# Kernel optimization log

Measured on AMD Instinct MI355X. Metric: run time of the kernel, lower is better.

## Reference

```python
import jax, jax.numpy as jnp
import numpy as np

N_QUBITS = 6
Q_DEPTH = 2
K = 3
PAD = 1
EPS = 1e-9
Q_DIM = 2 ** N_QUBITS


def _rx(t):
    c = jnp.cos(t / 2).astype(jnp.complex64)
    s = jnp.sin(t / 2).astype(jnp.complex64)
    return jnp.stack([jnp.stack([c, -1j * s]), jnp.stack([-1j * s, c])])


def _ry(t):
    c = jnp.cos(t / 2).astype(jnp.complex64)
    s = jnp.sin(t / 2).astype(jnp.complex64)
    return jnp.stack([jnp.stack([c, -s]), jnp.stack([s, c])])


def _u3(t, p, lm):
    c = jnp.cos(t / 2).astype(jnp.complex64)
    s = jnp.sin(t / 2).astype(jnp.complex64)
    ep = jnp.exp(1j * p.astype(jnp.complex64))
    el = jnp.exp(1j * lm.astype(jnp.complex64))
    return jnp.stack([jnp.stack([c, -el * s]), jnp.stack([ep * s, ep * el * c])])


def _apply_1q(st, U, wire):
    # st: (bsz, 2**n) complex; wire 0 = most significant bit (torchquantum layout)
    s = st.reshape(-1, 2 ** wire, 2, 2 ** (N_QUBITS - wire - 1))
    s = jnp.einsum('ab,nxby->nxay', U, s)
    return s.reshape(-1, Q_DIM)


def _apply_cnot(st, wire):
    # CNOT with control=wire, target=wire+1 (adjacent)
    s = st.reshape(-1, 2 ** wire, 2, 2, 2 ** (N_QUBITS - wire - 2))
    s = jnp.stack([s[:, :, 0], s[:, :, 1, ::-1]], axis=2)
    return s.reshape(-1, Q_DIM)


def _quantum_forward(x, inp_scale, in_proj_w, in_proj_b, weights, meas_w, out_proj_w, out_proj_b):
    B, C, H, W = x.shape
    # Unfold(kernel=3, pad=1, stride=1) -> (B, C*9, H*W), channel-major then (kh, kw)
    xp = jnp.pad(x, ((0, 0), (0, 0), (PAD, PAD), (PAD, PAD)))
    pat = jnp.stack([xp[:, :, i:i + H, j:j + W] for i in range(K) for j in range(K)], axis=2)
    pat = pat.reshape(B, C * K * K, H * W).transpose(0, 2, 1).reshape(-1, C * K * K)
    pf = pat * inp_scale
    xq = pf @ in_proj_w.T + in_proj_b                       # (bsz, 64)
    xq = xq / (jnp.linalg.norm(xq, axis=-1, keepdims=True) + EPS)
    st = xq.astype(jnp.complex64)                           # (bsz, 2**n)
    for l in range(Q_DEPTH):
        for i in range(N_QUBITS):
            st = _apply_1q(st, _rx(weights[l, i, 0]), i)
            st = _apply_1q(st, _ry(weights[l, i, 1]), i)
        for i in range(N_QUBITS - 1):
            st = _apply_cnot(st, i)
        for i in range(N_QUBITS):
            st = _apply_1q(st, _ry(weights[l, i, 2]), i)
    for i in range(N_QUBITS):
        st = _apply_1q(st, _u3(meas_w[i, 0], meas_w[i, 1], meas_w[i, 2]), i)
    probs = st.real ** 2 + st.imag ** 2                     # |amp|^2
    out = probs @ out_proj_w.T + out_proj_b                 # (bsz, out_channels)
    return out.reshape(B, H * W, -1).transpose(0, 2, 1).reshape(B, -1, H, W)


def setup_inputs() -> dict:
    key = jax.random.key(0)
    ks = jax.random.split(key, 8)
    C_IN, C_OUT = 32, 64
    patch_dim = C_IN * K * K  # 288
    x = jax.random.normal(ks[0], (16, C_IN, 64, 64), dtype=jnp.float32)
    inp_scale = jnp.ones((patch_dim,), dtype=jnp.float32)
    in_proj_w = jax.random.normal(ks[1], (Q_DIM, patch_dim), dtype=jnp.float32) / np.sqrt(patch_dim)
    in_proj_b = jax.random.normal(ks[2], (Q_DIM,), dtype=jnp.float32) / np.sqrt(patch_dim)
    weights = 0.1 * jax.random.normal(ks[3], (Q_DEPTH, N_QUBITS, 3), dtype=jnp.float32)
    meas_w = 0.1 * jax.random.normal(ks[4], (N_QUBITS, 3), dtype=jnp.float32)
    out_proj_w = jax.random.normal(ks[5], (C_OUT, Q_DIM), dtype=jnp.float32) / np.sqrt(Q_DIM)
    out_proj_b = jax.random.normal(ks[6], (C_OUT,), dtype=jnp.float32) / np.sqrt(Q_DIM)
    return {"x": x, "inp_scale": inp_scale, "in_proj_w": in_proj_w, "in_proj_b": in_proj_b,
            "weights": weights, "meas_w": meas_w, "out_proj_w": out_proj_w, "out_proj_b": out_proj_b}


def reference(x, inp_scale, in_proj_w, in_proj_b, weights, meas_w, out_proj_w, out_proj_b):
    return _quantum_forward(x, inp_scale, in_proj_w, in_proj_b, weights, meas_w, out_proj_w, out_proj_b)
```

## Files before the change

kernel.cpp:

```cpp
#include <hip/hip_runtime.h>

typedef float f32x4 __attribute__((ext_vector_type(4)));
typedef short bf16x8 __attribute__((ext_vector_type(8)));

#define NB   16
#define CIN  32
#define HW   64
#define CKK  288
#define QD   64

#define WS_WSF 0
#define WS_MCF 18432
#define WS_WOF 26624
#define WS_XQF 30720

__device__ __forceinline__ unsigned short f2bf(float f) {
  unsigned u = __builtin_bit_cast(unsigned, f);
  u += 0x7FFFu + ((u >> 16) & 1u);
  return (unsigned short)(u >> 16);
}

struct C2 { float r, i; };
struct M2 { C2 a, b, c, d; };

__device__ __forceinline__ C2 cmul(C2 x, C2 y) { return { x.r*y.r - x.i*y.i, x.r*y.i + x.i*y.r }; }
__device__ __forceinline__ C2 cadd(C2 x, C2 y) { return { x.r + y.r, x.i + y.i }; }
__device__ __forceinline__ M2 mmul(M2 X, M2 Y) {
  return { cadd(cmul(X.a, Y.a), cmul(X.b, Y.c)),
           cadd(cmul(X.a, Y.b), cmul(X.b, Y.d)),
           cadd(cmul(X.c, Y.a), cmul(X.d, Y.c)),
           cadd(cmul(X.c, Y.b), cmul(X.d, Y.d)) };
}

__device__ __forceinline__ M2 mRX(float t) {
  float s, c; __sincosf(t * 0.5f, &s, &c);
  return { {c,0.f}, {0.f,-s}, {0.f,-s}, {c,0.f} };
}
__device__ __forceinline__ M2 mRY(float t) {
  float s, c; __sincosf(t * 0.5f, &s, &c);
  return { {c,0.f}, {-s,0.f}, {s,0.f}, {c,0.f} };
}
__device__ __forceinline__ M2 mU3(float t, float p, float lm) {
  float s, c; __sincosf(t * 0.5f, &s, &c);
  float sp, cp; __sincosf(p, &sp, &cp);
  float sl, cl; __sincosf(lm, &sl, &cl);
  float spl, cpl; __sincosf(p + lm, &spl, &cpl);
  return { {c,0.f}, {-cl*s, -sl*s}, {cp*s, sp*s}, {cpl*c, spl*c} };
}

__global__ __launch_bounds__(256) void prep_kernel(
    const float* __restrict__ x,
    const float* __restrict__ in_proj_w, const float* __restrict__ inp_scale,
    const float* __restrict__ weights, const float* __restrict__ meas_w,
    const float* __restrict__ out_proj_w, unsigned short* __restrict__ ws)
{
  const int tid = threadIdx.x, blk = blockIdx.x;

  if (blk < 1024) {
    const int b = blk >> 6, y = blk & 63;
    const int lane = tid & 63, w = tid >> 6;
    const float* src = x + ((b * CIN + w * 8) * HW + y) * HW + lane;
    unsigned short* dst = ws + WS_XQF + (size_t)((b * HW + y) * HW + lane) * CIN + w * 8;
    bf16x8 o8;
#pragma unroll
    for (int j = 0; j < 8; ++j) o8[j] = (short)f2bf(src[j * HW * HW]);
    *(bf16x8*)dst = o8;
    return;
  }
  const int blk2 = blk - 1024;

  if (blk2 < 36) {
    int f = blk2, kk = f >> 2, jt = f & 3;
#pragma unroll
    for (int u = 0; u < 2; ++u) {
      int r = tid * 2 + u;
      int lw = r >> 3, e = r & 7;
      int row = jt * 16 + (lw & 15);
      int ch = (lw >> 4) * 8 + e;
      int src = ch * 9 + kk;
      ws[WS_WSF + f * 512 + r] = f2bf(in_proj_w[row * CKK + src] * inp_scale[src]);
    }
    return;
  }
  if (blk2 == 36) {
#pragma unroll
    for (int m = 0; m < 16; ++m) {
      int d = tid * 16 + m;
      int f = d >> 9, r = d & 511;
      int lw = r >> 3, e = r & 7;
      int kk = f >> 2, ot = f & 3;
      int src = (ot * 16 + (lw & 15)) * 64 + kk * 32 + (lw >> 4) * 8 + e;
      ws[WS_WOF + d] = f2bf(out_proj_w[src]);
    }
    return;
  }

  const int lane = tid & 63, wid = tid >> 6;
  const int col = (blk2 - 37) * 4 + wid;

  float re, im;
  {
    C2 amp = {1.f, 0.f};
#pragma unroll
    for (int q = 0; q < 6; ++q) {
      M2 G = mmul(mRY(weights[q * 3 + 1]), mRX(weights[q * 3 + 0]));
      int rb = (lane >> (5 - q)) & 1;
      int cb = (col >> (5 - q)) & 1;
      C2 sel = rb ? (cb ? G.d : G.c) : (cb ? G.b : G.a);
      amp = cmul(amp, sel);
    }
    re = amp.r; im = amp.i;
  }

  const int t1 = (lane ^ (lane >> 1) ^ (lane >> 2) ^ (lane >> 3) ^ (lane >> 4) ^ (lane >> 5)) & 63;
  const int t2 = (lane ^ (lane >> 2) ^ (lane >> 4)) & 63;

  auto applyM = [&](int maskShuf, int rb, M2 U) {
    float arr = rb ? U.d.r : U.a.r, ari = rb ? U.d.i : U.a.i;
    float brr = rb ? U.c.r : U.b.r, bri = rb ? U.c.i : U.b.i;
    float pre = __shfl_xor(re, maskShuf);
    float pim = __shfl_xor(im, maskShuf);
    float nr = arr * re - ari * im + brr * pre - bri * pim;
    float ni = arr * im + ari * re + brr * pim + bri * pre;
    re = nr; im = ni;
  };

  const int MK1[6] = {0x01, 0x03, 0x06, 0x0C, 0x18, 0x30};
  const int MK2[6] = {0x01, 0x02, 0x05, 0x0A, 0x14, 0x28};

#pragma unroll
  for (int q = 0; q < 6; ++q) {
    const int b = 5 - q;
    M2 U = mmul(mmul(mRY(weights[18 + q * 3 + 1]), mRX(weights[18 + q * 3 + 0])),
                mRY(weights[q * 3 + 2]));
    applyM(MK1[b], (t1 >> b) & 1, U);
  }
#pragma unroll
  for (int q = 0; q < 6; ++q) {
    const int b = 5 - q;
    M2 U = mmul(mU3(meas_w[q * 3], meas_w[q * 3 + 1], meas_w[q * 3 + 2]),
                mRY(weights[18 + q * 3 + 2]));
    applyM(MK2[b], (t2 >> b) & 1, U);
  }

  unsigned short* McF = ws + WS_MCF;
  const int nRe = t2 >> 4, c16r = t2 & 15;
  const int kk = col >> 5, gc = (col >> 3) & 3, e = col & 7;
  const int off = (gc * 16 + c16r) * 8 + e;
  McF[(kk * 8 + nRe) * 512 + off]     = f2bf(re);
  McF[(kk * 8 + 4 + nRe) * 512 + off] = f2bf(im);
}

#define LDA 72
#define LDO 65

__global__ __launch_bounds__(256) void main_kernel(
    const float* __restrict__ b_in, const float* __restrict__ b_out,
    const unsigned short* __restrict__ ws, float* __restrict__ out)
{
  __shared__ __align__(16) unsigned char smem[18432];
  unsigned short* a_lds = (unsigned short*)smem;
  unsigned short* p_lds = (unsigned short*)(smem + 9216);
  float* o_lds = (float*)smem;

  const int tid = threadIdx.x, lane = tid & 63, wid = tid >> 6;
  const int g = lane >> 4, c16 = lane & 15;
  const int blk = (blockIdx.x & 7) * 128 + (blockIdx.x >> 3);
  const int b = blk >> 6, h = blk & 63;

  const unsigned short* WsF = ws + WS_WSF;
  const unsigned short* McF = ws + WS_MCF;
  const unsigned short* WoF = ws + WS_WOF;
  const unsigned short* xqb = ws + WS_XQF + (size_t)b * (HW * HW * CIN);

  f32x4 acc[4];
#pragma unroll
  for (int jt = 0; jt < 4; ++jt) { float bi = b_in[jt * 16 + c16]; acc[jt] = f32x4{bi, bi, bi, bi}; }

  const int ar = wid * 16 + c16;
  const int xw0 = (ar >= 1) ? ar - 1 : 0;
  const int xw2 = (ar <= 62) ? ar + 1 : 63;
  const bool ok0 = (ar >= 1), ok2 = (ar <= 62);

#pragma unroll
  for (int kk = 0; kk < 9; ++kk) {
    const int di = kk / 3, dj = kk % 3;
    const int y = h + di - 1;
    bf16x8 af;
    if ((unsigned)y < 64u) {
      const int xwc = (dj == 0) ? xw0 : (dj == 1) ? ar : xw2;
      af = *(const bf16x8*)(xqb + (y * 64 + xwc) * CIN + g * 8);
      const bool okx = (dj == 0) ? ok0 : (dj == 1) ? true : ok2;
      if (!okx)
#pragma unroll
        for (int i = 0; i < 8; ++i) af[i] = 0;
    } else {
#pragma unroll
      for (int i = 0; i < 8; ++i) af[i] = 0;
    }
#pragma unroll
    for (int jt = 0; jt < 4; ++jt) {
      bf16x8 bf_ = *(const bf16x8*)(WsF + (kk * 4 + jt) * 512 + lane * 8);
      acc[jt] = __builtin_amdgcn_mfma_f32_16x16x32_bf16(af, bf_, acc[jt], 0, 0, 0);
    }
  }

  float s[4];
#pragma unroll
  for (int r = 0; r < 4; ++r) {
    float t = acc[0][r] * acc[0][r] + acc[1][r] * acc[1][r] +
              acc[2][r] * acc[2][r] + acc[3][r] * acc[3][r];
    t += __shfl_xor(t, 1); t += __shfl_xor(t, 2); t += __shfl_xor(t, 4); t += __shfl_xor(t, 8);
    s[r] = 1.f / (sqrtf(t) + 1e-9f);
  }
#pragma unroll
  for (int jt = 0; jt < 4; ++jt)
#pragma unroll
    for (int r = 0; r < 4; ++r)
      a_lds[(wid * 16 + g * 4 + r) * LDA + jt * 16 + c16] = f2bf(acc[jt][r] * s[r]);

  f32x4 uv[8];
#pragma unroll
  for (int n = 0; n < 8; ++n) uv[n] = f32x4{0.f, 0.f, 0.f, 0.f};
#pragma unroll
  for (int kk = 0; kk < 2; ++kk) {
    bf16x8 af = *(const bf16x8*)(a_lds + (wid * 16 + c16) * LDA + kk * 32 + g * 8);
#pragma unroll
    for (int n = 0; n < 8; ++n) {
      bf16x8 bf_ = *(const bf16x8*)(McF + (kk * 8 + n) * 512 + lane * 8);
      uv[n] = __builtin_amdgcn_mfma_f32_16x16x32_bf16(af, bf_, uv[n], 0, 0, 0);
    }
  }

#pragma unroll
  for (int n = 0; n < 4; ++n)
#pragma unroll
    for (int r = 0; r < 4; ++r) {
      float p = uv[n][r] * uv[n][r] + uv[n + 4][r] * uv[n + 4][r];
      p_lds[(wid * 16 + g * 4 + r) * LDA + n * 16 + c16] = f2bf(p);
    }

  f32x4 o[4];
#pragma unroll
  for (int ot = 0; ot < 4; ++ot) { float bo = b_out[ot * 16 + c16]; o[ot] = f32x4{bo, bo, bo, bo}; }
#pragma unroll
  for (int kk = 0; kk < 2; ++kk) {
    bf16x8 af = *(const bf16x8*)(p_lds + (wid * 16 + c16) * LDA + kk * 32 + g * 8);
#pragma unroll
    for (int ot = 0; ot < 4; ++ot) {
      bf16x8 bf_ = *(const bf16x8*)(WoF + (kk * 4 + ot) * 512 + lane * 8);
      o[ot] = __builtin_amdgcn_mfma_f32_16x16x32_bf16(af, bf_, o[ot], 0, 0, 0);
    }
  }

  __syncthreads();
#pragma unroll
  for (int ot = 0; ot < 4; ++ot)
#pragma unroll
    for (int r = 0; r < 4; ++r)
      o_lds[(ot * 16 + c16) * LDO + wid * 16 + g * 4 + r] = o[ot][r];
  __syncthreads();

  float* outb = out + (size_t)b * QD * HW * HW + h * HW;
#pragma unroll
  for (int it = 0; it < 16; ++it) {
    int orow = it * 4 + wid;
    outb[orow * (HW * HW) + lane] = o_lds[orow * LDO + lane];
  }
}

extern "C" void kernel_launch(void* const* d_in, const int* in_sizes, int n_in,
                              void* d_out, int out_size, void* d_ws, size_t ws_size,
                              hipStream_t stream) {
  const float* x          = (const float*)d_in[0];
  const float* inp_scale  = (const float*)d_in[1];
  const float* in_proj_w  = (const float*)d_in[2];
  const float* in_proj_b  = (const float*)d_in[3];
  const float* weights    = (const float*)d_in[4];
  const float* meas_w     = (const float*)d_in[5];
  const float* out_proj_w = (const float*)d_in[6];
  const float* out_proj_b = (const float*)d_in[7];
  unsigned short* ws = (unsigned short*)d_ws;

  prep_kernel<<<1077, 256, 0, stream>>>(x, in_proj_w, inp_scale, weights, meas_w, out_proj_w, ws);
  main_kernel<<<NB * HW, 256, 0, stream>>>(in_proj_b, out_proj_b, ws, (float*)d_out);
}
```

Baseline: 24.61 us.

## Stage weight matrices in LDS and process two rows per 512-thread block

The main kernel now uses 512-thread blocks that each cover two image rows. At block start it copies all three bf16 weight fragment sets (in-proj, circuit, out-proj) into shared memory, and the MFMA B operands are then read from LDS instead of global memory. The point is to cut repeated per-wave global/L1 weight traffic and amortize it across eight waves. In exchange, each block needs about 78 KB of LDS, which limits occupancy to roughly two blocks per CU, and every block pays an up-front copy plus a barrier. The output staging buffer reuses the weight region after the barrier.

```diff
diff --git a/kernel.cpp b/kernel.cpp
--- a/kernel.cpp
+++ b/kernel.cpp
@@ -12,6 +12,7 @@
 #define WS_WSF 0
 #define WS_MCF 18432
 #define WS_WOF 26624
+#define WS_WEND 30720
 #define WS_XQF 30720
 
 __device__ __forceinline__ unsigned short f2bf(float f) {
@@ -154,30 +155,38 @@
 #define LDA 72
 #define LDO 65
 
-__global__ __launch_bounds__(256) void main_kernel(
+__global__ __launch_bounds__(512, 4) void main_kernel(
     const float* __restrict__ b_in, const float* __restrict__ b_out,
     const unsigned short* __restrict__ ws, float* __restrict__ out)
 {
-  __shared__ __align__(16) unsigned char smem[18432];
-  unsigned short* a_lds = (unsigned short*)smem;
-  unsigned short* p_lds = (unsigned short*)(smem + 9216);
+  __shared__ __align__(16) unsigned char smem[79872];
+  unsigned short* w_lds = (unsigned short*)smem;
+  unsigned short* a_lds = (unsigned short*)(smem + 61440);
   float* o_lds = (float*)smem;
 
   const int tid = threadIdx.x, lane = tid & 63, wid = tid >> 6;
   const int g = lane >> 4, c16 = lane & 15;
-  const int blk = (blockIdx.x & 7) * 128 + (blockIdx.x >> 3);
-  const int b = blk >> 6, h = blk & 63;
-
-  const unsigned short* WsF = ws + WS_WSF;
-  const unsigned short* McF = ws + WS_MCF;
-  const unsigned short* WoF = ws + WS_WOF;
+  const int blk = ((int)blockIdx.x & 7) * 64 + ((int)blockIdx.x >> 3);
+  const int b = blk >> 5, h0 = (blk & 31) * 2;
+  const int hloc = wid >> 2;
+  const int h = h0 + hloc;
+
+  for (int c = tid; c < 3840; c += 512) {
+    bf16x8 v = *(const bf16x8*)(ws + c * 8);
+    *(bf16x8*)(w_lds + c * 8) = v;
+  }
+  __syncthreads();
+
+  const unsigned short* WsL = w_lds + WS_WSF;
+  const unsigned short* McL = w_lds + WS_MCF;
+  const unsigned short* WoL = w_lds + WS_WOF;
   const unsigned short* xqb = ws + WS_XQF + (size_t)b * (HW * HW * CIN);
 
   f32x4 acc[4];
 #pragma unroll
   for (int jt = 0; jt < 4; ++jt) { float bi = b_in[jt * 16 + c16]; acc[jt] = f32x4{bi, bi, bi, bi}; }
 
-  const int ar = wid * 16 + c16;
+  const int ar = (wid & 3) * 16 + c16;
   const int xw0 = (ar >= 1) ? ar - 1 : 0;
   const int xw2 = (ar <= 62) ? ar + 1 : 63;
   const bool ok0 = (ar >= 1), ok2 = (ar <= 62);
@@ -200,7 +209,7 @@
     }
 #pragma unroll
     for (int jt = 0; jt < 4; ++jt) {
-      bf16x8 bf_ = *(const bf16x8*)(WsF + (kk * 4 + jt) * 512 + lane * 8);
+      bf16x8 bf_ = *(const bf16x8*)(WsL + (kk * 4 + jt) * 512 + lane * 8);
       acc[jt] = __builtin_amdgcn_mfma_f32_16x16x32_bf16(af, bf_, acc[jt], 0, 0, 0);
     }
   }
@@ -227,7 +236,7 @@
     bf16x8 af = *(const bf16x8*)(a_lds + (wid * 16 + c16) * LDA + kk * 32 + g * 8);
 #pragma unroll
     for (int n = 0; n < 8; ++n) {
-      bf16x8 bf_ = *(const bf16x8*)(McF + (kk * 8 + n) * 512 + lane * 8);
+      bf16x8 bf_ = *(const bf16x8*)(McL + (kk * 8 + n) * 512 + lane * 8);
       uv[n] = __builtin_amdgcn_mfma_f32_16x16x32_bf16(af, bf_, uv[n], 0, 0, 0);
     }
   }
@@ -237,7 +246,7 @@
 #pragma unroll
     for (int r = 0; r < 4; ++r) {
       float p = uv[n][r] * uv[n][r] + uv[n + 4][r] * uv[n + 4][r];
-      p_lds[(wid * 16 + g * 4 + r) * LDA + n * 16 + c16] = f2bf(p);
+      a_lds[(wid * 16 + g * 4 + r) * LDA + n * 16 + c16] = f2bf(p);
     }
 
   f32x4 o[4];
@@ -245,10 +254,10 @@
   for (int ot = 0; ot < 4; ++ot) { float bo = b_out[ot * 16 + c16]; o[ot] = f32x4{bo, bo, bo, bo}; }
 #pragma unroll
   for (int kk = 0; kk < 2; ++kk) {
-    bf16x8 af = *(const bf16x8*)(p_lds + (wid * 16 + c16) * LDA + kk * 32 + g * 8);
+    bf16x8 af = *(const bf16x8*)(a_lds + (wid * 16 + c16) * LDA + kk * 32 + g * 8);
 #pragma unroll
     for (int ot = 0; ot < 4; ++ot) {
-      bf16x8 bf_ = *(const bf16x8*)(WoF + (kk * 4 + ot) * 512 + lane * 8);
+      bf16x8 bf_ = *(const bf16x8*)(WoL + (kk * 4 + ot) * 512 + lane * 8);
       o[ot] = __builtin_amdgcn_mfma_f32_16x16x32_bf16(af, bf_, o[ot], 0, 0, 0);
     }
   }
@@ -258,14 +267,15 @@
   for (int ot = 0; ot < 4; ++ot)
 #pragma unroll
     for (int r = 0; r < 4; ++r)
-      o_lds[(ot * 16 + c16) * LDO + wid * 16 + g * 4 + r] = o[ot][r];
+      o_lds[hloc * (QD * LDO) + (ot * 16 + c16) * LDO + (wid & 3) * 16 + g * 4 + r] = o[ot][r];
   __syncthreads();
 
-  float* outb = out + (size_t)b * QD * HW * HW + h * HW;
+  float* outb = out + (size_t)b * QD * HW * HW + h0 * HW;
 #pragma unroll
   for (int it = 0; it < 16; ++it) {
-    int orow = it * 4 + wid;
-    outb[orow * (HW * HW) + lane] = o_lds[orow * LDO + lane];
+    int r2 = it * 8 + wid;
+    int orow = r2 >> 1, hl = r2 & 1;
+    outb[orow * (HW * HW) + hl * HW + lane] = o_lds[hl * (QD * LDO) + orow * LDO + lane];
   }
 }
 
@@ -283,5 +293,5 @@
   unsigned short* ws = (unsigned short*)d_ws;
 
   prep_kernel<<<1077, 256, 0, stream>>>(x, in_proj_w, inp_scale, weights, meas_w, out_proj_w, ws);
-  main_kernel<<<NB * HW, 256, 0, stream>>>(in_proj_b, out_proj_b, ws, (float*)d_out);
-}
+  main_kernel<<<512, 512, 0, stream>>>(in_proj_b, out_proj_b, ws, (float*)d_out);
+}
```

Result: faster. 22.32 us (-9.3%).
